# Kernel tuning notes

Hardware: AMD Instinct MI355X
Metric: run time of the kernel (lower is better)

Reference implementation:

```python
import jax, jax.numpy as jnp
import numpy as np

B, T, D = 4, 4096, 256
N_SCALES, N_EXPERTS = 3, 4
KERNELS = [5, 9, 17]           # kernel bank, one group of N_EXPERTS experts per size
E = N_SCALES * N_EXPERTS       # 12 total experts
EPS = 1e-5


def _dw_causal_conv(x, w):
    """Depthwise causal conv over time. x:[B,T,D], w:[k,D] -> [B,T,D]."""
    k = w.shape[0]
    xp = jnp.pad(x, ((0, 0), (k - 1, 0), (0, 0)))
    return jax.lax.conv_general_dilated(
        xp, w[:, None, :], window_strides=(1,), padding='VALID',
        dimension_numbers=('NWC', 'WIO', 'NWC'), feature_group_count=x.shape[-1])


def setup_inputs() -> dict:
    key = jax.random.key(0)
    ks = jax.random.split(key, 12)
    s = 0.02
    return {
        'x':       jax.random.normal(ks[0], (B, T, D), jnp.float32),
        'conv_k5':  jax.random.normal(ks[1], (N_EXPERTS, 5, D), jnp.float32) * s,
        'conv_k9':  jax.random.normal(ks[2], (N_EXPERTS, 9, D), jnp.float32) * s,
        'conv_k17': jax.random.normal(ks[3], (N_EXPERTS, 17, D), jnp.float32) * s,
        'proj_W':   jax.random.normal(ks[4], (E, D, D), jnp.float32) * s,
        'proj_b':   jnp.zeros((E, D), jnp.float32),
        'router_W': jax.random.normal(ks[5], (D, E), jnp.float32) * s,
        'router_b': jnp.zeros((E,), jnp.float32),
        'out_W':    jax.random.normal(ks[6], (D, D), jnp.float32) * s,
        'out_b':    jnp.zeros((D,), jnp.float32),
        'gamma':    jnp.ones((D,), jnp.float32),
        'beta':     jnp.zeros((D,), jnp.float32),
    }


def reference(x, conv_k5, conv_k9, conv_k17, proj_W, proj_b,
              router_W, router_b, out_W, out_b, gamma, beta):
    # per-scale expert SSM (causal depthwise conv), vmapped over the 4 experts per size
    ssm_out = jnp.concatenate([
        jax.vmap(lambda w: _dw_causal_conv(x, w))(conv_k5),
        jax.vmap(lambda w: _dw_causal_conv(x, w))(conv_k9),
        jax.vmap(lambda w: _dw_causal_conv(x, w))(conv_k17),
    ], axis=0)                                             # [E,B,T,D]
    # per-expert linear projection -> [B,T,E,D]
    stack = jnp.einsum('ebtd,edf->btef', ssm_out, proj_W) + proj_b
    # router: convex combination over E experts per token
    weights = jax.nn.softmax(x @ router_W + router_b, axis=-1)   # [B,T,E]
    mixed = jnp.einsum('btef,bte->btf', stack, weights)          # [B,T,D]
    # LayerNorm
    mu = jnp.mean(mixed, axis=-1, keepdims=True)
    var = jnp.var(mixed, axis=-1, keepdims=True)
    normed = (mixed - mu) * jax.lax.rsqrt(var + EPS) * gamma + beta
    return normed @ out_W + out_b
```

## Files before the change

kernel.cpp:

```cpp
#include <hip/hip_runtime.h>
#include <hip/hip_bf16.h>

typedef short short8 __attribute__((ext_vector_type(8)));
typedef short short4_t __attribute__((ext_vector_type(4)));
typedef float floatx4 __attribute__((ext_vector_type(4)));

#define DEVI __device__ __forceinline__


DEVI float bf2f(__hip_bfloat16 v) { return __bfloat162float(v); }
DEVI __hip_bfloat16 f2bf(float v) { return __float2bfloat16(v); }
DEVI unsigned short bfbits(float v) { __hip_bfloat16 b = f2bf(v); return *(unsigned short*)&b; }

__global__ __launch_bounds__(256) void prep_kernel(
    const float* __restrict__ rW,
    const float* __restrict__ projW,
    const float* __restrict__ outW,
    const float* __restrict__ projb,
    __hip_bfloat16* __restrict__ projWT,
    __hip_bfloat16* __restrict__ outWT,
    __hip_bfloat16* __restrict__ projbT,
    __hip_bfloat16* __restrict__ rWT)
{
    __shared__ __align__(16) __hip_bfloat16 Tt[64 * 72];
    const int bid = blockIdx.x;
    const int tid = threadIdx.x;

    if (bid == 208) {
#pragma unroll
        for (int k = 0; k < 32; k++)
            projbT[tid * 32 + k] = (k < 12) ? f2bf(projb[k * 256 + tid]) : f2bf(0.f);
#pragma unroll
        for (int e = 0; e < 16; e++)
            rWT[e * 256 + tid] = (e < 12) ? f2bf(rW[tid * 12 + e]) : f2bf(0.f);
        return;
    }
    const float* src;
    __hip_bfloat16* dst;
    if (bid < 192) {
        int e = bid >> 4, ti = (bid & 15) >> 2, tj = bid & 3;
        src = projW + (e << 16) + (ti * 64) * 256 + tj * 64;
        dst = projWT + (e << 16) + (tj * 64) * 256 + ti * 64;
    } else {
        int b3 = bid - 192, ti = b3 >> 2, tj = b3 & 3;
        src = outW + (ti * 64) * 256 + tj * 64;
        dst = outWT + (tj * 64) * 256 + ti * 64;
    }
#pragma unroll
    for (int i = 0; i < 4; i++) {
        int r = i * 16 + (tid >> 4);
        int c4 = (tid & 15) * 4;
        float4 f = *(const float4*)(src + r * 256 + c4);
        Tt[(c4 + 0) * 72 + r] = f2bf(f.x);
        Tt[(c4 + 1) * 72 + r] = f2bf(f.y);
        Tt[(c4 + 2) * 72 + r] = f2bf(f.z);
        Tt[(c4 + 3) * 72 + r] = f2bf(f.w);
    }
    __syncthreads();
#pragma unroll
    for (int i = 0; i < 2; i++) {
        int c = i * 32 + (tid >> 3);
        int r8 = (tid & 7) * 8;
        *(short8*)(dst + c * 256 + r8) = *(const short8*)(Tt + c * 72 + r8);
    }
}


template<int K>
DEVI void conv_lds(const float (&c)[17],
                   const __hip_bfloat16* __restrict__ xs,
                   int tloc,
                   const float* __restrict__ wts_s, int e,
                   __hip_bfloat16* __restrict__ dst, int d_l, int d_g)
{
    float w[K - 1];
#pragma unroll
    for (int i = 0; i < K - 1; i++)
        w[i] = bf2f(xs[(16 + tloc - (K - 1) + i) * 264 + d_g]);
#pragma unroll
    for (int t = 0; t < 16; t++) {
        float nv = bf2f(xs[(16 + tloc + t) * 264 + d_g]);
        float s = nv * c[K - 1];
#pragma unroll
        for (int i = 0; i < K - 1; i++) s += w[i] * c[i];
        dst[(tloc + t) * 136 + d_l] = f2bf(s * wts_s[(tloc + t) * 12 + e]);
#pragma unroll
        for (int i = 0; i + 1 < K - 1; i++) w[i] = w[i + 1];
        w[K - 2] = nv;
    }
}

template<int NKS>
DEVI void gemm_pre(const __hip_bfloat16* __restrict__ A,
                   const short8 (&B)[4][2], floatx4 (&acc)[4][2],
                   int l16, int quad)
{
    const __hip_bfloat16* ap = A + l16 * 136 + quad * 8;
    short8 a[4];
#pragma unroll
    for (int mf = 0; mf < 4; mf++) a[mf] = *(const short8*)(ap + mf * 16 * 136);
#pragma unroll
    for (int ks = 0; ks < NKS; ks++) {
        short8 na[4];
        if (ks < NKS - 1) {
#pragma unroll
            for (int mf = 0; mf < 4; mf++)
                na[mf] = *(const short8*)(ap + mf * 16 * 136 + (ks + 1) * 32);
        }
#pragma unroll
        for (int nt = 0; nt < 2; nt++)
#pragma unroll
            for (int mf = 0; mf < 4; mf++)
                acc[mf][nt] = __builtin_amdgcn_mfma_f32_16x16x32_bf16(
                    a[mf], B[ks][nt], acc[mf][nt], 0, 0, 0);
        if (ks < NKS - 1) {
#pragma unroll
            for (int mf = 0; mf < 4; mf++) a[mf] = na[mf];
        }
    }
}

DEVI void gemm_out(const __hip_bfloat16* __restrict__ A,
                   const __hip_bfloat16* __restrict__ Bg,
                   floatx4 (&acc)[4][2], int l16, int quad, int nsl)
{
    const __hip_bfloat16* ap = A + l16 * 264 + quad * 8;
    const __hip_bfloat16* bp = Bg + (nsl + l16) * 256 + quad * 8;
    short8 a[4], b[2];
#pragma unroll
    for (int mf = 0; mf < 4; mf++) a[mf] = *(const short8*)(ap + mf * 16 * 264);
#pragma unroll
    for (int nt = 0; nt < 2; nt++) b[nt] = *(const short8*)(bp + nt * 16 * 256);
#pragma unroll
    for (int ks = 0; ks < 8; ks++) {
        short8 na[4], nb[2];
        if (ks < 7) {
#pragma unroll
            for (int mf = 0; mf < 4; mf++)
                na[mf] = *(const short8*)(ap + mf * 16 * 264 + (ks + 1) * 32);
#pragma unroll
            for (int nt = 0; nt < 2; nt++)
                nb[nt] = *(const short8*)(bp + nt * 16 * 256 + (ks + 1) * 32);
        }
#pragma unroll
        for (int nt = 0; nt < 2; nt++)
#pragma unroll
            for (int mf = 0; mf < 4; mf++)
                acc[mf][nt] = __builtin_amdgcn_mfma_f32_16x16x32_bf16(
                    a[mf], b[nt], acc[mf][nt], 0, 0, 0);
        if (ks < 7) {
#pragma unroll
            for (int mf = 0; mf < 4; mf++) a[mf] = na[mf];
#pragma unroll
            for (int nt = 0; nt < 2; nt++) b[nt] = nb[nt];
        }
    }
}

__global__ __launch_bounds__(512, 1) void fused_kernel(
    const float* __restrict__ x,
    const float* __restrict__ ck5, const float* __restrict__ ck9,
    const float* __restrict__ ck17,
    const float* __restrict__ rb,
    const float* __restrict__ gmm, const float* __restrict__ bta,
    const float* __restrict__ outb,
    const __hip_bfloat16* __restrict__ projWT,
    const __hip_bfloat16* __restrict__ outWT,
    const __hip_bfloat16* __restrict__ projbT,
    const __hip_bfloat16* __restrict__ rWT,
    float* __restrict__ out)
{
    __shared__ __align__(16) char smem[62720];
    __hip_bfloat16* xs = (__hip_bfloat16*)smem;
    __hip_bfloat16* As = (__hip_bfloat16*)(smem + 42240);
    float* wts_s = (float*)(smem + 59648);
    __hip_bfloat16* normed = (__hip_bfloat16*)smem;
    float* psum = (float*)(smem + 33792);
    float* psq  = (float*)(smem + 36096);
    float* muA  = (float*)(smem + 38400);
    float* rsA  = (float*)(smem + 38656);

    const int tid  = threadIdx.x;
    const int wave = tid >> 6;
    const int lane = tid & 63;
    const int quad = lane >> 4;
    const int l16  = lane & 15;
    const int nsl  = wave * 32;
    const int m0   = blockIdx.x * 64;
    const int bb   = m0 >> 12;
    const int t0   = m0 & 4095;

    {
        const float* xb = x + (size_t)bb * 4096 * 256;
        for (int idx = tid; idx < 80 * 64; idx += 512) {
            int row = idx >> 6, c4 = (idx & 63) << 2;
            int gt = t0 - 16 + row;
            short4_t v = {0, 0, 0, 0};
            if (gt >= 0) {
                float4 f = *(const float4*)(xb + (size_t)gt * 256 + c4);
                v[0] = (short)bfbits(f.x); v[1] = (short)bfbits(f.y);
                v[2] = (short)bfbits(f.z); v[3] = (short)bfbits(f.w);
            }
            *(short4_t*)(xs + row * 264 + c4) = v;
        }
    }
    __syncthreads();

    if (wave < 4) {
        floatx4 ra = {0.f, 0.f, 0.f, 0.f};
        const __hip_bfloat16* ap = xs + (16 + wave * 16 + l16) * 264 + quad * 8;
        const __hip_bfloat16* bp = rWT + l16 * 256 + quad * 8;
#pragma unroll
        for (int kk = 0; kk < 256; kk += 32)
            ra = __builtin_amdgcn_mfma_f32_16x16x32_bf16(
                *(const short8*)(ap + kk), *(const short8*)(bp + kk), ra, 0, 0, 0);
        float rbv = (l16 < 12) ? rb[l16] : 0.f;
#pragma unroll
        for (int r = 0; r < 4; r++) {
            float v = (l16 < 12) ? (ra[r] + rbv) : -1e30f;
            float mx = v;
            mx = fmaxf(mx, __shfl_xor(mx, 1));
            mx = fmaxf(mx, __shfl_xor(mx, 2));
            mx = fmaxf(mx, __shfl_xor(mx, 4));
            mx = fmaxf(mx, __shfl_xor(mx, 8));
            float ex = (l16 < 12) ? __expf(v - mx) : 0.f;
            float sm = ex;
            sm += __shfl_xor(sm, 1);
            sm += __shfl_xor(sm, 2);
            sm += __shfl_xor(sm, 4);
            sm += __shfl_xor(sm, 8);
            if (l16 < 12) wts_s[(wave * 16 + quad * 4 + r) * 12 + l16] = ex / sm;
        }
    }
    __syncthreads();

    auto loadCoef = [&](float (&cr)[17], int c) {
        int e = c >> 1;
        int d_g = (c & 1) * 128 + (tid & 127);
        if (e < 4) {
            const float* cw = ck5 + e * 5 * 256;
#pragma unroll
            for (int j = 0; j < 17; j++) cr[j] = (j < 5) ? cw[j * 256 + d_g] : 0.f;
        } else if (e < 8) {
            const float* cw = ck9 + (e - 4) * 9 * 256;
#pragma unroll
            for (int j = 0; j < 17; j++) cr[j] = (j < 9) ? cw[j * 256 + d_g] : 0.f;
        } else {
            const float* cw = ck17 + (e - 8) * 17 * 256;
#pragma unroll
            for (int j = 0; j < 17; j++) cr[j] = cw[j * 256 + d_g];
        }
    };
    auto loadB = [&](short8 (&B)[4][2], int c) {
        const __hip_bfloat16* bp;
        int rs, kstep;
        if (c < 24) {
            int e = c >> 1, h = c & 1;
            bp = projWT + (e << 16) + h * 128 + (nsl + l16) * 256 + quad * 8;
            rs = 256; kstep = 32;
        } else {
            bp = projbT + (nsl + l16) * 32 + quad * 8;
            rs = 32; kstep = 0;
        }
#pragma unroll
        for (int ks = 0; ks < 4; ks++)
#pragma unroll
            for (int nt = 0; nt < 2; nt++)
                B[ks][nt] = *(const short8*)(bp + nt * 16 * rs + ks * kstep);
    };
    auto produce = [&](int c, const float (&cr)[17]) {
        if (c == 24) {
            int t = tid >> 3, k4 = (tid & 7) * 4;
            short4_t v;
#pragma unroll
            for (int j = 0; j < 4; j++) {
                int k = k4 + j;
                v[j] = (k < 12) ? (short)bfbits(wts_s[t * 12 + k]) : (short)0;
            }
            *(short4_t*)(As + t * 136 + k4) = v;
        } else {
            int e = c >> 1;
            int d_l = tid & 127, tloc = (tid >> 7) * 16;
            int d_g = (c & 1) * 128 + d_l;
            if (e < 4)
                conv_lds<5>(cr, xs, tloc, wts_s, e, As, d_l, d_g);
            else if (e < 8)
                conv_lds<9>(cr, xs, tloc, wts_s, e, As, d_l, d_g);
            else
                conv_lds<17>(cr, xs, tloc, wts_s, e, As, d_l, d_g);
        }
    };

    floatx4 acc[4][2];
#pragma unroll
    for (int i = 0; i < 4; i++)
#pragma unroll
        for (int j = 0; j < 2; j++) acc[i][j] = {0.f, 0.f, 0.f, 0.f};

    float crA[17], crB[17];
    short8 BA[4][2], BB[4][2];

    loadB(BA, 0);
    loadCoef(crA, 0);
    produce(0, crA);
    __syncthreads();

#pragma unroll 1
    for (int cc = 0; cc < 12; cc++) {
        int c0 = 2 * cc;
        loadCoef(crB, c0 + 1);
        loadB(BB, c0 + 1);
        gemm_pre<4>(As, BA, acc, l16, quad);
        __syncthreads();
        produce(c0 + 1, crB);
        __syncthreads();
        if (c0 + 2 < 24) loadCoef(crA, c0 + 2);
        loadB(BA, c0 + 2);
        gemm_pre<4>(As, BB, acc, l16, quad);
        __syncthreads();
        produce(c0 + 2, crA);
        __syncthreads();
    }
    gemm_pre<1>(As, BA, acc, l16, quad);

    {
        float s[16], s2[16];
#pragma unroll
        for (int mf = 0; mf < 4; mf++)
#pragma unroll
            for (int r = 0; r < 4; r++) {
                int i = mf * 4 + r;
                float v = 0.f, q = 0.f;
#pragma unroll
                for (int nt = 0; nt < 2; nt++) {
                    float a = acc[mf][nt][r];
                    v += a; q += a * a;
                }
                s[i] = v; s2[i] = q;
            }
#pragma unroll
        for (int m = 1; m <= 8; m <<= 1)
#pragma unroll
            for (int i = 0; i < 16; i++) {
                s[i]  += __shfl_xor(s[i], m);
                s2[i] += __shfl_xor(s2[i], m);
            }
#pragma unroll
        for (int i = 0; i < 16; i++)
            if (l16 == i) {
                int row = (i >> 2) * 16 + quad * 4 + (i & 3);
                psum[row * 9 + wave] = s[i];
                psq[row * 9 + wave]  = s2[i];
            }
    }
    __syncthreads();
    if (tid < 64) {
        float ss = 0.f, qq = 0.f;
#pragma unroll
        for (int p = 0; p < 8; p++) { ss += psum[tid * 9 + p]; qq += psq[tid * 9 + p]; }
        float mu = ss * 0.00390625f;
        float var = fmaxf(qq * 0.00390625f - mu * mu, 0.f);
        muA[tid] = mu;
        rsA[tid] = rsqrtf(var + 1e-5f);
    }
    __syncthreads();

#pragma unroll
    for (int nt = 0; nt < 2; nt++) {
        int col = nsl + nt * 16 + l16;
        float g = gmm[col], bt = bta[col];
#pragma unroll
        for (int mf = 0; mf < 4; mf++)
#pragma unroll
            for (int r = 0; r < 4; r++) {
                int row = mf * 16 + quad * 4 + r;
                normed[row * 264 + col] =
                    f2bf((acc[mf][nt][r] - muA[row]) * rsA[row] * g + bt);
            }
    }
    __syncthreads();

    floatx4 acc2[4][2];
#pragma unroll
    for (int i = 0; i < 4; i++)
#pragma unroll
        for (int j = 0; j < 2; j++) acc2[i][j] = {0.f, 0.f, 0.f, 0.f};
    gemm_out(normed, outWT, acc2, l16, quad, nsl);

    float* op = out + (size_t)m0 * 256;
#pragma unroll
    for (int nt = 0; nt < 2; nt++) {
        int col = nsl + nt * 16 + l16;
        float ob = outb[col];
#pragma unroll
        for (int mf = 0; mf < 4; mf++)
#pragma unroll
            for (int r = 0; r < 4; r++) {
                int row = mf * 16 + quad * 4 + r;
                op[row * 256 + col] = acc2[mf][nt][r] + ob;
            }
    }
}

extern "C" void kernel_launch(void* const* d_in, const int* in_sizes, int n_in,
                              void* d_out, int out_size, void* d_ws, size_t ws_size,
                              hipStream_t stream)
{
    (void)in_sizes; (void)n_in; (void)out_size; (void)ws_size;
    const float* x     = (const float*)d_in[0];
    const float* ck5   = (const float*)d_in[1];
    const float* ck9   = (const float*)d_in[2];
    const float* ck17  = (const float*)d_in[3];
    const float* projW = (const float*)d_in[4];
    const float* projb = (const float*)d_in[5];
    const float* rW    = (const float*)d_in[6];
    const float* rb    = (const float*)d_in[7];
    const float* outW  = (const float*)d_in[8];
    const float* outb  = (const float*)d_in[9];
    const float* gmm   = (const float*)d_in[10];
    const float* bta   = (const float*)d_in[11];

    __hip_bfloat16* projWT = (__hip_bfloat16*)d_ws;
    __hip_bfloat16* outWT  = (__hip_bfloat16*)((char*)d_ws + 1572864);
    __hip_bfloat16* projbT = (__hip_bfloat16*)((char*)d_ws + 1703936);
    __hip_bfloat16* rWT    = (__hip_bfloat16*)((char*)d_ws + 1720320);

    prep_kernel<<<dim3(209), dim3(256), 0, stream>>>(
        rW, projW, outW, projb, projWT, outWT, projbT, rWT);
    fused_kernel<<<dim3(256), dim3(512), 0, stream>>>(
        x, ck5, ck9, ck17, rb, gmm, bta, outb,
        projWT, outWT, projbT, rWT, (float*)d_out);
}
```

Before: 164.1 us.

## Hold conv input window in registers and process full expert per stage

```diff
diff --git a/kernel.cpp b/kernel.cpp
--- a/kernel.cpp
+++ b/kernel.cpp
@@ -67,45 +67,41 @@
 
 
 template<int K>
-DEVI void conv_lds(const float (&c)[17],
-                   const __hip_bfloat16* __restrict__ xs,
-                   int tloc,
-                   const float* __restrict__ wts_s, int e,
-                   __hip_bfloat16* __restrict__ dst, int d_l, int d_g)
-{
-    float w[K - 1];
-#pragma unroll
-    for (int i = 0; i < K - 1; i++)
-        w[i] = bf2f(xs[(16 + tloc - (K - 1) + i) * 264 + d_g]);
+DEVI void conv_reg(const float2 (&cf)[17], const unsigned (&xr)[32],
+                   const float4 (&wt4)[4], unsigned* __restrict__ dp)
+{
+    constexpr int OFF = 17 - K;
 #pragma unroll
     for (int t = 0; t < 16; t++) {
-        float nv = bf2f(xs[(16 + tloc + t) * 264 + d_g]);
-        float s = nv * c[K - 1];
-#pragma unroll
-        for (int i = 0; i < K - 1; i++) s += w[i] * c[i];
-        dst[(tloc + t) * 136 + d_l] = f2bf(s * wts_s[(tloc + t) * 12 + e]);
-#pragma unroll
-        for (int i = 0; i + 1 < K - 1; i++) w[i] = w[i + 1];
-        w[K - 2] = nv;
+        float y0 = 0.f, y1 = 0.f;
+#pragma unroll
+        for (int i = 0; i < K; i++) {
+            unsigned u = xr[t + OFF + i];
+            y0 = fmaf(cf[i].x, __uint_as_float(u << 16), y0);
+            y1 = fmaf(cf[i].y, __uint_as_float(u & 0xffff0000u), y1);
+        }
+        float wt = wt4[t >> 2][t & 3];
+        unsigned pv = ((unsigned)bfbits(y1 * wt) << 16) | (unsigned)bfbits(y0 * wt);
+        dp[t * 132] = pv;
     }
 }
 
 template<int NKS>
-DEVI void gemm_pre(const __hip_bfloat16* __restrict__ A,
+DEVI void gemm_pre(const __hip_bfloat16* __restrict__ A, int astride,
                    const short8 (&B)[4][2], floatx4 (&acc)[4][2],
                    int l16, int quad)
 {
-    const __hip_bfloat16* ap = A + l16 * 136 + quad * 8;
+    const __hip_bfloat16* ap = A + l16 * astride + quad * 8;
     short8 a[4];
 #pragma unroll
-    for (int mf = 0; mf < 4; mf++) a[mf] = *(const short8*)(ap + mf * 16 * 136);
+    for (int mf = 0; mf < 4; mf++) a[mf] = *(const short8*)(ap + mf * 16 * astride);
 #pragma unroll
     for (int ks = 0; ks < NKS; ks++) {
         short8 na[4];
         if (ks < NKS - 1) {
 #pragma unroll
             for (int mf = 0; mf < 4; mf++)
-                na[mf] = *(const short8*)(ap + mf * 16 * 136 + (ks + 1) * 32);
+                na[mf] = *(const short8*)(ap + mf * 16 * astride + (ks + 1) * 32);
         }
 #pragma unroll
         for (int nt = 0; nt < 2; nt++)
@@ -116,43 +112,6 @@
         if (ks < NKS - 1) {
 #pragma unroll
             for (int mf = 0; mf < 4; mf++) a[mf] = na[mf];
-        }
-    }
-}
-
-DEVI void gemm_out(const __hip_bfloat16* __restrict__ A,
-                   const __hip_bfloat16* __restrict__ Bg,
-                   floatx4 (&acc)[4][2], int l16, int quad, int nsl)
-{
-    const __hip_bfloat16* ap = A + l16 * 264 + quad * 8;
-    const __hip_bfloat16* bp = Bg + (nsl + l16) * 256 + quad * 8;
-    short8 a[4], b[2];
-#pragma unroll
-    for (int mf = 0; mf < 4; mf++) a[mf] = *(const short8*)(ap + mf * 16 * 264);
-#pragma unroll
-    for (int nt = 0; nt < 2; nt++) b[nt] = *(const short8*)(bp + nt * 16 * 256);
-#pragma unroll
-    for (int ks = 0; ks < 8; ks++) {
-        short8 na[4], nb[2];
-        if (ks < 7) {
-#pragma unroll
-            for (int mf = 0; mf < 4; mf++)
-                na[mf] = *(const short8*)(ap + mf * 16 * 264 + (ks + 1) * 32);
-#pragma unroll
-            for (int nt = 0; nt < 2; nt++)
-                nb[nt] = *(const short8*)(bp + nt * 16 * 256 + (ks + 1) * 32);
-        }
-#pragma unroll
-        for (int nt = 0; nt < 2; nt++)
-#pragma unroll
-            for (int mf = 0; mf < 4; mf++)
-                acc[mf][nt] = __builtin_amdgcn_mfma_f32_16x16x32_bf16(
-                    a[mf], b[nt], acc[mf][nt], 0, 0, 0);
-        if (ks < 7) {
-#pragma unroll
-            for (int mf = 0; mf < 4; mf++) a[mf] = na[mf];
-#pragma unroll
-            for (int nt = 0; nt < 2; nt++) b[nt] = nb[nt];
         }
     }
 }
@@ -170,15 +129,15 @@
     const __hip_bfloat16* __restrict__ rWT,
     float* __restrict__ out)
 {
-    __shared__ __align__(16) char smem[62720];
+    __shared__ __align__(16) char smem[50432];
     __hip_bfloat16* xs = (__hip_bfloat16*)smem;
-    __hip_bfloat16* As = (__hip_bfloat16*)(smem + 42240);
-    float* wts_s = (float*)(smem + 59648);
+    __hip_bfloat16* As = (__hip_bfloat16*)smem;
     __hip_bfloat16* normed = (__hip_bfloat16*)smem;
-    float* psum = (float*)(smem + 33792);
-    float* psq  = (float*)(smem + 36096);
-    float* muA  = (float*)(smem + 38400);
-    float* rsA  = (float*)(smem + 38656);
+    float* wts_s = (float*)(smem + 42240);
+    float* psum  = (float*)(smem + 45312);
+    float* psq   = (float*)(smem + 47616);
+    float* muA   = (float*)(smem + 49920);
+    float* rsA   = (float*)(smem + 50176);
 
     const int tid  = threadIdx.x;
     const int wave = tid >> 6;
@@ -229,99 +188,100 @@
             sm += __shfl_xor(sm, 2);
             sm += __shfl_xor(sm, 4);
             sm += __shfl_xor(sm, 8);
-            if (l16 < 12) wts_s[(wave * 16 + quad * 4 + r) * 12 + l16] = ex / sm;
-        }
-    }
-    __syncthreads();
-
-    auto loadCoef = [&](float (&cr)[17], int c) {
-        int e = c >> 1;
-        int d_g = (c & 1) * 128 + (tid & 127);
+            if (l16 < 12) wts_s[l16 * 64 + (wave * 16 + quad * 4 + r)] = ex / sm;
+        }
+    }
+
+    const int d0   = 2 * (tid & 127);
+    const int tloc = (tid >> 7) * 16;
+    unsigned xr[32];
+#pragma unroll
+    for (int j = 0; j < 32; j++)
+        xr[j] = *(const unsigned*)(xs + (tloc + j) * 264 + d0);
+    __syncthreads();
+
+    auto loadCoef = [&](float2 (&cf)[17], int e) {
         if (e < 4) {
             const float* cw = ck5 + e * 5 * 256;
 #pragma unroll
-            for (int j = 0; j < 17; j++) cr[j] = (j < 5) ? cw[j * 256 + d_g] : 0.f;
+            for (int j = 0; j < 17; j++)
+                cf[j] = (j < 5) ? *(const float2*)(cw + j * 256 + d0) : make_float2(0.f, 0.f);
         } else if (e < 8) {
             const float* cw = ck9 + (e - 4) * 9 * 256;
 #pragma unroll
-            for (int j = 0; j < 17; j++) cr[j] = (j < 9) ? cw[j * 256 + d_g] : 0.f;
+            for (int j = 0; j < 17; j++)
+                cf[j] = (j < 9) ? *(const float2*)(cw + j * 256 + d0) : make_float2(0.f, 0.f);
         } else {
             const float* cw = ck17 + (e - 8) * 17 * 256;
 #pragma unroll
-            for (int j = 0; j < 17; j++) cr[j] = cw[j * 256 + d_g];
+            for (int j = 0; j < 17; j++)
+                cf[j] = *(const float2*)(cw + j * 256 + d0);
         }
     };
-    auto loadB = [&](short8 (&B)[4][2], int c) {
-        const __hip_bfloat16* bp;
-        int rs, kstep;
-        if (c < 24) {
-            int e = c >> 1, h = c & 1;
-            bp = projWT + (e << 16) + h * 128 + (nsl + l16) * 256 + quad * 8;
-            rs = 256; kstep = 32;
+    auto loadB8 = [&](short8 (&B)[4][2], const __hip_bfloat16* base, int rs, int kstep) {
+#pragma unroll
+        for (int ks = 0; ks < 4; ks++)
+#pragma unroll
+            for (int nt = 0; nt < 2; nt++)
+                B[ks][nt] = *(const short8*)(base + nt * 16 * rs + ks * kstep);
+    };
+    auto produce = [&](int e, const float2 (&cf)[17]) {
+        float4 wt4[4];
+#pragma unroll
+        for (int g = 0; g < 4; g++)
+            wt4[g] = *(const float4*)(wts_s + e * 64 + tloc + 4 * g);
+        unsigned* dp = (unsigned*)As + tloc * 132 + (d0 >> 1);
+        if (e < 4)      conv_reg<5>(cf, xr, wt4, dp);
+        else if (e < 8) conv_reg<9>(cf, xr, wt4, dp);
+        else            conv_reg<17>(cf, xr, wt4, dp);
+    };
+    auto produceBias = [&]() {
+        int t = tid >> 3, k4 = (tid & 7) * 4;
+        short4_t v;
+#pragma unroll
+        for (int j = 0; j < 4; j++) {
+            int k = k4 + j;
+            v[j] = (k < 12) ? (short)bfbits(wts_s[k * 64 + t]) : (short)0;
+        }
+        *(short4_t*)(As + t * 264 + k4) = v;
+    };
+
+    floatx4 acc[4][2];
+#pragma unroll
+    for (int i = 0; i < 4; i++)
+#pragma unroll
+        for (int j = 0; j < 2; j++) acc[i][j] = {0.f, 0.f, 0.f, 0.f};
+
+    float2 cf[17];
+    short8 BA[4][2], BB[4][2];
+
+    loadCoef(cf, 0);
+    loadB8(BA, projWT + (0 << 16) + 0   + (nsl + l16) * 256 + quad * 8, 256, 32);
+    loadB8(BB, projWT + (0 << 16) + 128 + (nsl + l16) * 256 + quad * 8, 256, 32);
+    produce(0, cf);
+    __syncthreads();
+
+#pragma unroll 1
+    for (int c = 0; c < 12; c++) {
+        if (c < 11) loadCoef(cf, c + 1);
+        gemm_pre<4>(As, 264, BA, acc, l16, quad);
+        gemm_pre<4>(As + 128, 264, BB, acc, l16, quad);
+        if (c < 11) {
+            int e = c + 1;
+            loadB8(BA, projWT + (e << 16) + 0   + (nsl + l16) * 256 + quad * 8, 256, 32);
+            loadB8(BB, projWT + (e << 16) + 128 + (nsl + l16) * 256 + quad * 8, 256, 32);
         } else {
-            bp = projbT + (nsl + l16) * 32 + quad * 8;
-            rs = 32; kstep = 0;
-        }
-#pragma unroll
-        for (int ks = 0; ks < 4; ks++)
-#pragma unroll
-            for (int nt = 0; nt < 2; nt++)
-                B[ks][nt] = *(const short8*)(bp + nt * 16 * rs + ks * kstep);
-    };
-    auto produce = [&](int c, const float (&cr)[17]) {
-        if (c == 24) {
-            int t = tid >> 3, k4 = (tid & 7) * 4;
-            short4_t v;
-#pragma unroll
-            for (int j = 0; j < 4; j++) {
-                int k = k4 + j;
-                v[j] = (k < 12) ? (short)bfbits(wts_s[t * 12 + k]) : (short)0;
-            }
-            *(short4_t*)(As + t * 136 + k4) = v;
-        } else {
-            int e = c >> 1;
-            int d_l = tid & 127, tloc = (tid >> 7) * 16;
-            int d_g = (c & 1) * 128 + d_l;
-            if (e < 4)
-                conv_lds<5>(cr, xs, tloc, wts_s, e, As, d_l, d_g);
-            else if (e < 8)
-                conv_lds<9>(cr, xs, tloc, wts_s, e, As, d_l, d_g);
-            else
-                conv_lds<17>(cr, xs, tloc, wts_s, e, As, d_l, d_g);
-        }
-    };
-
-    floatx4 acc[4][2];
-#pragma unroll
-    for (int i = 0; i < 4; i++)
-#pragma unroll
-        for (int j = 0; j < 2; j++) acc[i][j] = {0.f, 0.f, 0.f, 0.f};
-
-    float crA[17], crB[17];
-    short8 BA[4][2], BB[4][2];
-
-    loadB(BA, 0);
-    loadCoef(crA, 0);
-    produce(0, crA);
-    __syncthreads();
-
-#pragma unroll 1
-    for (int cc = 0; cc < 12; cc++) {
-        int c0 = 2 * cc;
-        loadCoef(crB, c0 + 1);
-        loadB(BB, c0 + 1);
-        gemm_pre<4>(As, BA, acc, l16, quad);
+            loadB8(BA, projbT + (nsl + l16) * 32 + quad * 8, 32, 0);
+        }
         __syncthreads();
-        produce(c0 + 1, crB);
+        if (c < 11) produce(c + 1, cf);
+        else        produceBias();
         __syncthreads();
-        if (c0 + 2 < 24) loadCoef(crA, c0 + 2);
-        loadB(BA, c0 + 2);
-        gemm_pre<4>(As, BB, acc, l16, quad);
-        __syncthreads();
-        produce(c0 + 2, crA);
-        __syncthreads();
-    }
-    gemm_pre<1>(As, BA, acc, l16, quad);
+    }
+    gemm_pre<1>(As, 264, BA, acc, l16, quad);
+
+    loadB8(BA, outWT + 0   + (nsl + l16) * 256 + quad * 8, 256, 32);
+    loadB8(BB, outWT + 128 + (nsl + l16) * 256 + quad * 8, 256, 32);
 
     {
         float s[16], s2[16];
@@ -385,7 +345,8 @@
     for (int i = 0; i < 4; i++)
 #pragma unroll
         for (int j = 0; j < 2; j++) acc2[i][j] = {0.f, 0.f, 0.f, 0.f};
-    gemm_out(normed, outWT, acc2, l16, quad, nsl);
+    gemm_pre<4>(normed, 264, BA, acc2, l16, quad);
+    gemm_pre<4>(normed + 128, 264, BB, acc2, l16, quad);
 
     float* op = out + (size_t)m0 * 256;
 #pragma unroll
```

After: 165.6 us. No clear change (+0.9%).
